# Performance work log

Hardware: AMD Instinct MI355X
Metric: run time of the kernel (lower is better)

Reference implementation:

```python
import jax, jax.numpy as jnp
import numpy as np

SIZE = 1024
CODE_DIM = 256
B, H, W = 32, 32, 32


def setup_inputs() -> dict:
    key = jax.random.key(0)
    k1, k2 = jax.random.split(key)
    z = jax.random.normal(k1, (B, CODE_DIM, H, W), dtype=jnp.float32)
    embeddings = jax.random.normal(k2, (SIZE, CODE_DIM), dtype=jnp.float32)
    return {"z": z, "embeddings": embeddings}


def reference(z, embeddings):
    b, c, h, w = z.shape  # c == code_dim
    # (b, h, w, c) -> (N, c)
    flat = jnp.transpose(z, (0, 2, 3, 1)).reshape(-1, c)
    d = (
        jnp.sum(flat * flat, axis=-1, keepdims=True)
        - 2.0 * (flat @ embeddings.T)
        + jnp.sum(embeddings * embeddings, axis=-1)
    )
    idx = jnp.argmin(d, axis=-1)  # (N,)
    quantized = embeddings[idx].reshape(b, h, w, c)
    quantized = jnp.transpose(quantized, (0, 3, 1, 2))  # (b, c, h, w)
    straight_through = jax.lax.stop_gradient(quantized - z) + z
    return quantized, straight_through, idx.reshape(b, h, w)
```

## Files before the change

### kernel.cpp

```cpp
#include <hip/hip_runtime.h>

#define NPTS   32768
#define NCODES 1024
#define DIM    256
#define HWSZ   1024
#define CHW    (DIM*HWSZ)
#define QSZ    8388608

typedef __attribute__((ext_vector_type(8))) short short8;
typedef __attribute__((ext_vector_type(4))) float f32x4;

__device__ __forceinline__ void gload16(const void* g, void* l) {
    __builtin_amdgcn_global_load_lds((const __attribute__((address_space(1))) void*)g,
                                     (__attribute__((address_space(3))) void*)l,
                                     16, 0, 0);
}

__device__ __forceinline__ unsigned bf16_rne(float f) {
    unsigned u = __float_as_uint(f);
    return (u + 0x7fffu + ((u >> 16) & 1u)) >> 16;
}

__device__ __forceinline__ unsigned long long pack_di(float d, int code) {
    unsigned u = __float_as_uint(d);
    unsigned key = u ^ ((unsigned)((int)u >> 31) | 0x80000000u);
    return ((unsigned long long)key << 32) | (unsigned)code;
}

__device__ __forceinline__ int fmoff(int n, int c) {
    return ((((((n >> 7) * 2 + ((n >> 6) & 1)) * 8 + (c >> 5)) * 4 + ((n >> 4) & 3)) * 4
             + ((c >> 3) & 3)) * 16 + (n & 15)) * 8 + (c & 7);
}

__global__ void k_prep(const float* __restrict__ z, const float* __restrict__ emb,
                       short* __restrict__ Xh, short* __restrict__ Xl,
                       short* __restrict__ Eh, short* __restrict__ El,
                       float* __restrict__ e2, unsigned long long* __restrict__ win) {
    int tid = threadIdx.x;
    if (blockIdx.x >= 2048) {
        int eb = blockIdx.x - 2048;
        int widx = eb * 256 + tid;
        if (widx < NPTS) win[widx] = ~0ull;
        int lane = tid & 63, w = tid >> 6;
        int k = eb * 4 + w;
        const float4 v = *reinterpret_cast<const float4*>(emb + k * DIM + lane * 4);
        float f[4] = {v.x, v.y, v.z, v.w};
        short h[4], l[4];
        double s = 0.0;
        #pragma unroll
        for (int i = 0; i < 4; ++i) {
            unsigned hb = bf16_rne(f[i]);
            float hf = __uint_as_float(hb << 16);
            h[i] = (short)hb;
            l[i] = (short)bf16_rne(f[i] - hf);
            s += (double)f[i] * f[i];
        }
        int eoff = fmoff(k, lane * 4);
        *reinterpret_cast<short4*>(Eh + eoff) = make_short4(h[0], h[1], h[2], h[3]);
        *reinterpret_cast<short4*>(El + eoff) = make_short4(l[0], l[1], l[2], l[3]);
        #pragma unroll
        for (int m = 32; m >= 1; m >>= 1) s += __shfl_xor(s, m);
        if (lane == 0) e2[k] = (float)s;
        return;
    }
    __shared__ float T[64][33];
    int blk = blockIdx.x;
    int b   = blk >> 6;
    int rem = blk & 63;
    int ht  = rem >> 1;
    int ch  = rem & 1;
    int hw0 = ht * 32;
    int n0  = b * HWSZ + hw0;
    int hq = tid & 7, cr = tid >> 3;
    int wp = tid >> 3, wc = tid & 7;
    const float* zp = z + b * CHW;
    #pragma unroll
    for (int cc2 = 0; cc2 < 2; ++cc2) {
        int c0 = (ch * 2 + cc2) * 64;
        if (cc2) __syncthreads();
        #pragma unroll
        for (int p = 0; p < 2; ++p) {
            int c = p * 32 + cr;
            float4 v = *reinterpret_cast<const float4*>(zp + (c0 + c) * HWSZ + hw0 + hq * 4);
            T[c][hq * 4 + 0] = v.x; T[c][hq * 4 + 1] = v.y;
            T[c][hq * 4 + 2] = v.z; T[c][hq * 4 + 3] = v.w;
        }
        __syncthreads();
        short8 hv, lv;
        #pragma unroll
        for (int k = 0; k < 8; ++k) {
            float f = T[wc * 8 + k][wp];
            unsigned hb = bf16_rne(f);
            float hf = __uint_as_float(hb << 16);
            hv[k] = (short)hb;
            lv[k] = (short)bf16_rne(f - hf);
        }
        int off = fmoff(n0 + wp, c0 + wc * 8);
        *reinterpret_cast<short8*>(Xh + off) = hv;
        *reinterpret_cast<short8*>(Xl + off) = lv;
    }
}

__launch_bounds__(256, 3)
__global__ void k_dist(const short* __restrict__ Xh, const short* __restrict__ Xl,
                       const short* __restrict__ Eh, const short* __restrict__ El,
                       const float* __restrict__ e2, unsigned long long* __restrict__ win) {
    __shared__ __align__(16) short Bs[2][8192];
    __shared__ float sv[2][128];
    __shared__ int   si[2][128];

    const int tid = threadIdx.x;
    const int pt = blockIdx.x & 255;
    const int ct = blockIdx.x >> 8;
    const int n0 = pt * 128;
    const int c0 = ct * 128;

    const int w = tid >> 6, lane = tid & 63;
    const int wr = w >> 1, wc = w & 1;
    const int m16 = lane & 15, quad = lane >> 4;

    f32x4 acc[4][4];
    #pragma unroll
    for (int i = 0; i < 4; ++i)
        #pragma unroll
        for (int j = 0; j < 4; ++j) acc[i][j] = (f32x4){0.f, 0.f, 0.f, 0.f};

    const short* Ahb = Xh + (pt * 2 + wr) * 16384 + lane * 8;
    const short* Alb = Xl + (pt * 2 + wr) * 16384 + lane * 8;
    const short* Ebase = (w < 2 ? Eh : El) + (ct * 2 + wc) * 16384 + lane * 8;
    char* BsW0 = (char*)&Bs[0][0] + w * 4096;
    char* BsW1 = (char*)&Bs[1][0] + w * 4096;

    #define STAGE_B(buf, tt) do {                                       \
        char* d_ = (buf) ? BsW1 : BsW0;                                 \
        const short* s_ = Ebase + (tt) * 2048;                          \
        gload16(s_,        d_);                                         \
        gload16(s_ + 512,  d_ + 1024);                                  \
        gload16(s_ + 1024, d_ + 2048);                                  \
        gload16(s_ + 1536, d_ + 3072);                                  \
    } while (0)

    short8 ah[2][4], al[4];
    STAGE_B(0, 0);
    #pragma unroll
    for (int i = 0; i < 4; ++i)
        ah[0][i] = *reinterpret_cast<const short8*>(Ahb + i * 512);

    #pragma unroll
    for (int t = 0; t < 8; ++t) {
        const int cur = t & 1;
        __builtin_amdgcn_s_barrier();
        #pragma unroll
        for (int i = 0; i < 4; ++i)
            al[i] = *reinterpret_cast<const short8*>(Alb + t * 2048 + i * 512);
        if (t < 7) STAGE_B(cur ^ 1, t + 1);
        if (t < 7) asm volatile("s_waitcnt vmcnt(8)" ::: "memory");
        else       asm volatile("s_waitcnt vmcnt(4)" ::: "memory");
        __builtin_amdgcn_sched_barrier(0);

        short8 bh[4];
        #pragma unroll
        for (int j = 0; j < 4; ++j)
            bh[j] = *(const short8*)&Bs[cur][(wc * 4 + j) * 512 + lane * 8];
        #pragma unroll
        for (int i = 0; i < 4; ++i)
            #pragma unroll
            for (int j = 0; j < 4; ++j)
                acc[i][j] = __builtin_amdgcn_mfma_f32_16x16x32_bf16(ah[cur][i], bh[j], acc[i][j], 0, 0, 0);
        #pragma unroll
        for (int i = 0; i < 4; ++i)
            #pragma unroll
            for (int j = 0; j < 4; ++j)
                acc[i][j] = __builtin_amdgcn_mfma_f32_16x16x32_bf16(al[i], bh[j], acc[i][j], 0, 0, 0);
        if (t < 7) {
            #pragma unroll
            for (int i = 0; i < 4; ++i)
                ah[cur ^ 1][i] = *reinterpret_cast<const short8*>(Ahb + (t + 1) * 2048 + i * 512);
        }
        short8 bl[4];
        #pragma unroll
        for (int j = 0; j < 4; ++j)
            bl[j] = *(const short8*)&Bs[cur][(8 + wc * 4 + j) * 512 + lane * 8];
        #pragma unroll
        for (int i = 0; i < 4; ++i)
            #pragma unroll
            for (int j = 0; j < 4; ++j)
                acc[i][j] = __builtin_amdgcn_mfma_f32_16x16x32_bf16(ah[cur][i], bl[j], acc[i][j], 0, 0, 0);
    }
    #undef STAGE_B

    float ecol[4];
    #pragma unroll
    for (int j = 0; j < 4; ++j) ecol[j] = e2[c0 + wc * 64 + j * 16 + m16];

    #pragma unroll
    for (int i = 0; i < 4; ++i) {
        #pragma unroll
        for (int rr = 0; rr < 4; ++rr) {
            float best = 3.4e38f; int bi = 0;
            #pragma unroll
            for (int j = 0; j < 4; ++j) {
                float d = fmaf(-2.f, acc[i][j][rr], ecol[j]);
                int code = c0 + wc * 64 + j * 16 + m16;
                if (d < best) { best = d; bi = code; }
            }
            #pragma unroll
            for (int m = 1; m < 16; m <<= 1) {
                float ov = __shfl_xor(best, m);
                int   oi = __shfl_xor(bi, m);
                if (ov < best || (ov == best && oi < bi)) { best = ov; bi = oi; }
            }
            if (m16 == 0) {
                int p = wr * 64 + i * 16 + quad * 4 + rr;
                sv[wc][p] = best; si[wc][p] = bi;
            }
        }
    }
    __syncthreads();
    if (tid < 128) {
        float v0 = sv[0][tid]; int i0 = si[0][tid];
        float v1 = sv[1][tid]; int i1 = si[1][tid];
        if (v1 < v0) { v0 = v1; i0 = i1; }
        atomicMin(win + n0 + tid, pack_di(v0, i0));
    }
}

__global__ void k_out(const float* __restrict__ z, const float* __restrict__ emb,
                      const unsigned long long* __restrict__ win,
                      float* __restrict__ out) {
    __shared__ float Q[32][129];
    __shared__ int sbi[32];
    int blk = blockIdx.x;
    int n0 = (blk >> 1) * 32;
    int ch = blk & 1;
    int tid = threadIdx.x;
    if (tid < 32) {
        int n = n0 + tid;
        int bi = (int)(unsigned)(win[n] & 0xFFFFFFFFull);
        sbi[tid] = bi;
        if (ch == 0) out[2 * QSZ + n] = (float)bi;
    }
    __syncthreads();
    {
        int pt = tid >> 3, co = tid & 7;
        const float* ep = emb + sbi[pt] * DIM + ch * 128;
        #pragma unroll
        for (int j = 0; j < 4; ++j) {
            int c = j * 32 + co * 4;
            float4 v = *reinterpret_cast<const float4*>(ep + c);
            Q[pt][c] = v.x; Q[pt][c + 1] = v.y; Q[pt][c + 2] = v.z; Q[pt][c + 3] = v.w;
        }
    }
    __syncthreads();
    int hq = tid & 7, cr = tid >> 3;
    int b = n0 >> 10, hw0 = (n0 & 1023) + hq * 4;
    #pragma unroll
    for (int it = 0; it < 4; ++it) {
        int cl = it * 32 + cr;
        int c  = ch * 128 + cl;
        int off = b * CHW + c * HWSZ + hw0;
        float4 zv = *reinterpret_cast<const float4*>(z + off);
        float4 q = make_float4(Q[hq * 4 + 0][cl], Q[hq * 4 + 1][cl],
                               Q[hq * 4 + 2][cl], Q[hq * 4 + 3][cl]);
        *reinterpret_cast<float4*>(out + off) = q;
        float4 st = make_float4((q.x - zv.x) + zv.x, (q.y - zv.y) + zv.y,
                                (q.z - zv.z) + zv.z, (q.w - zv.w) + zv.w);
        *reinterpret_cast<float4*>(out + QSZ + off) = st;
    }
}

extern "C" void kernel_launch(void* const* d_in, const int* in_sizes, int n_in,
                              void* d_out, int out_size, void* d_ws, size_t ws_size,
                              hipStream_t stream) {
    const float* z   = (const float*)d_in[0];
    const float* emb = (const float*)d_in[1];
    float* out = (float*)d_out;
    float* ws  = (float*)d_ws;

    short* Eh   = (short*)ws;
    short* El   = (short*)(ws + 131072);
    float* e2   = ws + 262144;
    unsigned long long* win = (unsigned long long*)(ws + 263168);

    short* Xh = (short*)out;
    short* Xl = (short*)(out + 4194304);

    hipLaunchKernelGGL(k_prep, dim3(2304), dim3(256), 0, stream, z, emb, Xh, Xl, Eh, El, e2, win);
    hipLaunchKernelGGL(k_dist, dim3(2048), dim3(256), 0, stream, Xh, Xl, Eh, El, e2, win);
    hipLaunchKernelGGL(k_out,  dim3(2048), dim3(256), 0, stream, z, emb, win, out);
}
```

Baseline: 165.8 us.

## Switch distance GEMM to 32x32x16 MFMA with matching fragment layout

Measured after the change: 194.7 us. +17.4%, slower.

```diff
diff --git a/kernel.cpp b/kernel.cpp
--- a/kernel.cpp
+++ b/kernel.cpp
@@ -8,7 +8,7 @@
 #define QSZ    8388608
 
 typedef __attribute__((ext_vector_type(8))) short short8;
-typedef __attribute__((ext_vector_type(4))) float f32x4;
+typedef __attribute__((ext_vector_type(16))) float f32x16;
 
 __device__ __forceinline__ void gload16(const void* g, void* l) {
     __builtin_amdgcn_global_load_lds((const __attribute__((address_space(1))) void*)g,
@@ -27,9 +27,8 @@
     return ((unsigned long long)key << 32) | (unsigned)code;
 }
 
-__device__ __forceinline__ int fmoff(int n, int c) {
-    return ((((((n >> 7) * 2 + ((n >> 6) & 1)) * 8 + (c >> 5)) * 4 + ((n >> 4) & 3)) * 4
-             + ((c >> 3) & 3)) * 16 + (n & 15)) * 8 + (c & 7);
+__device__ __forceinline__ int fmoff32(int n, int c) {
+    return ((n >> 5) * 16 + (c >> 4)) * 512 + (((c >> 3) & 1) * 32 + (n & 31)) * 8 + (c & 7);
 }
 
 __global__ void k_prep(const float* __restrict__ z, const float* __restrict__ emb,
@@ -55,7 +54,7 @@
             l[i] = (short)bf16_rne(f[i] - hf);
             s += (double)f[i] * f[i];
         }
-        int eoff = fmoff(k, lane * 4);
+        int eoff = fmoff32(k, lane * 4);
         *reinterpret_cast<short4*>(Eh + eoff) = make_short4(h[0], h[1], h[2], h[3]);
         *reinterpret_cast<short4*>(El + eoff) = make_short4(l[0], l[1], l[2], l[3]);
         #pragma unroll
@@ -95,7 +94,7 @@
             hv[k] = (short)hb;
             lv[k] = (short)bf16_rne(f - hf);
         }
-        int off = fmoff(n0 + wp, c0 + wc * 8);
+        int off = fmoff32(n0 + wp, c0 + wc * 8);
         *reinterpret_cast<short8*>(Xh + off) = hv;
         *reinterpret_cast<short8*>(Xl + off) = lv;
     }
@@ -117,101 +116,121 @@
 
     const int w = tid >> 6, lane = tid & 63;
     const int wr = w >> 1, wc = w & 1;
-    const int m16 = lane & 15, quad = lane >> 4;
-
-    f32x4 acc[4][4];
-    #pragma unroll
-    for (int i = 0; i < 4; ++i)
-        #pragma unroll
-        for (int j = 0; j < 4; ++j) acc[i][j] = (f32x4){0.f, 0.f, 0.f, 0.f};
-
-    const short* Ahb = Xh + (pt * 2 + wr) * 16384 + lane * 8;
-    const short* Alb = Xl + (pt * 2 + wr) * 16384 + lane * 8;
-    const short* Ebase = (w < 2 ? Eh : El) + (ct * 2 + wc) * 16384 + lane * 8;
-    char* BsW0 = (char*)&Bs[0][0] + w * 4096;
-    char* BsW1 = (char*)&Bs[1][0] + w * 4096;
-
-    #define STAGE_B(buf, tt) do {                                       \
-        char* d_ = (buf) ? BsW1 : BsW0;                                 \
-        const short* s_ = Ebase + (tt) * 2048;                          \
-        gload16(s_,        d_);                                         \
-        gload16(s_ + 512,  d_ + 1024);                                  \
-        gload16(s_ + 1024, d_ + 2048);                                  \
-        gload16(s_ + 1536, d_ + 3072);                                  \
+    const int l31 = lane & 31, lh = lane >> 5;
+
+    f32x16 acc[2][2];
+    #pragma unroll
+    for (int i = 0; i < 2; ++i)
+        #pragma unroll
+        for (int j = 0; j < 2; ++j)
+            #pragma unroll
+            for (int e = 0; e < 16; ++e) acc[i][j][e] = 0.f;
+
+    const short* Ahb = Xh + (pt * 4 + wr * 2) * 8192 + lane * 8;
+    const short* Alb = Xl + (pt * 4 + wr * 2) * 8192 + lane * 8;
+    const short* Ebase = (w < 2 ? Eh : El) + (ct * 4 + (w & 1) * 2) * 8192 + lane * 8;
+    char* Bd0 = (char*)&Bs[0][0] + ((w >> 1) * 8 + (w & 1) * 4) * 1024;
+    char* Bd1 = (char*)&Bs[1][0] + ((w >> 1) * 8 + (w & 1) * 4) * 1024;
+
+    #define STAGE_B(buf, tt) do {                                     \
+        char* d_ = (buf) ? Bd1 : Bd0;                                 \
+        const short* s_ = Ebase + (tt) * 1024;                        \
+        gload16(s_,              d_);                                 \
+        gload16(s_ + 512,        d_ + 1024);                          \
+        gload16(s_ + 8192,       d_ + 2048);                          \
+        gload16(s_ + 8192 + 512, d_ + 3072);                          \
     } while (0)
 
     short8 ah[2][4], al[4];
     STAGE_B(0, 0);
-    #pragma unroll
-    for (int i = 0; i < 4; ++i)
-        ah[0][i] = *reinterpret_cast<const short8*>(Ahb + i * 512);
+    __builtin_amdgcn_sched_barrier(0);
+    #pragma unroll
+    for (int f = 0; f < 4; ++f)
+        ah[0][f] = *reinterpret_cast<const short8*>(Ahb + (f >> 1) * 8192 + (f & 1) * 512);
+    asm volatile("s_waitcnt vmcnt(4)" ::: "memory");
+    __builtin_amdgcn_s_barrier();
+    __builtin_amdgcn_sched_barrier(0);
 
     #pragma unroll
     for (int t = 0; t < 8; ++t) {
         const int cur = t & 1;
-        __builtin_amdgcn_s_barrier();
-        #pragma unroll
-        for (int i = 0; i < 4; ++i)
-            al[i] = *reinterpret_cast<const short8*>(Alb + t * 2048 + i * 512);
+        short8 bh[4];
+        #pragma unroll
+        for (int f = 0; f < 4; ++f)
+            bh[f] = *(const short8*)&Bs[cur][(wc * 4 + f) * 512 + lane * 8];
+        #pragma unroll
+        for (int f = 0; f < 4; ++f)
+            al[f] = *reinterpret_cast<const short8*>(Alb + (f >> 1) * 8192 + (t * 2 + (f & 1)) * 512);
         if (t < 7) STAGE_B(cur ^ 1, t + 1);
-        if (t < 7) asm volatile("s_waitcnt vmcnt(8)" ::: "memory");
-        else       asm volatile("s_waitcnt vmcnt(4)" ::: "memory");
-        __builtin_amdgcn_sched_barrier(0);
-
-        short8 bh[4];
-        #pragma unroll
-        for (int j = 0; j < 4; ++j)
-            bh[j] = *(const short8*)&Bs[cur][(wc * 4 + j) * 512 + lane * 8];
-        #pragma unroll
-        for (int i = 0; i < 4; ++i)
-            #pragma unroll
-            for (int j = 0; j < 4; ++j)
-                acc[i][j] = __builtin_amdgcn_mfma_f32_16x16x32_bf16(ah[cur][i], bh[j], acc[i][j], 0, 0, 0);
-        #pragma unroll
-        for (int i = 0; i < 4; ++i)
-            #pragma unroll
-            for (int j = 0; j < 4; ++j)
-                acc[i][j] = __builtin_amdgcn_mfma_f32_16x16x32_bf16(al[i], bh[j], acc[i][j], 0, 0, 0);
+
+        __builtin_amdgcn_s_setprio(1);
+        #pragma unroll
+        for (int i2 = 0; i2 < 2; ++i2)
+            #pragma unroll
+            for (int j2 = 0; j2 < 2; ++j2)
+                #pragma unroll
+                for (int kf = 0; kf < 2; ++kf)
+                    acc[i2][j2] = __builtin_amdgcn_mfma_f32_32x32x16_bf16(
+                        ah[cur][i2 * 2 + kf], bh[j2 * 2 + kf], acc[i2][j2], 0, 0, 0);
+        #pragma unroll
+        for (int i2 = 0; i2 < 2; ++i2)
+            #pragma unroll
+            for (int j2 = 0; j2 < 2; ++j2)
+                #pragma unroll
+                for (int kf = 0; kf < 2; ++kf)
+                    acc[i2][j2] = __builtin_amdgcn_mfma_f32_32x32x16_bf16(
+                        al[i2 * 2 + kf], bh[j2 * 2 + kf], acc[i2][j2], 0, 0, 0);
+        __builtin_amdgcn_s_setprio(0);
         if (t < 7) {
-            #pragma unroll
-            for (int i = 0; i < 4; ++i)
-                ah[cur ^ 1][i] = *reinterpret_cast<const short8*>(Ahb + (t + 1) * 2048 + i * 512);
+            __builtin_amdgcn_sched_barrier(0);
+            #pragma unroll
+            for (int f = 0; f < 4; ++f)
+                ah[cur ^ 1][f] = *reinterpret_cast<const short8*>(
+                    Ahb + (f >> 1) * 8192 + ((t + 1) * 2 + (f & 1)) * 512);
         }
         short8 bl[4];
         #pragma unroll
-        for (int j = 0; j < 4; ++j)
-            bl[j] = *(const short8*)&Bs[cur][(8 + wc * 4 + j) * 512 + lane * 8];
-        #pragma unroll
-        for (int i = 0; i < 4; ++i)
-            #pragma unroll
-            for (int j = 0; j < 4; ++j)
-                acc[i][j] = __builtin_amdgcn_mfma_f32_16x16x32_bf16(ah[cur][i], bl[j], acc[i][j], 0, 0, 0);
+        for (int f = 0; f < 4; ++f)
+            bl[f] = *(const short8*)&Bs[cur][(8 + wc * 4 + f) * 512 + lane * 8];
+        __builtin_amdgcn_s_setprio(1);
+        #pragma unroll
+        for (int i2 = 0; i2 < 2; ++i2)
+            #pragma unroll
+            for (int j2 = 0; j2 < 2; ++j2)
+                #pragma unroll
+                for (int kf = 0; kf < 2; ++kf)
+                    acc[i2][j2] = __builtin_amdgcn_mfma_f32_32x32x16_bf16(
+                        ah[cur][i2 * 2 + kf], bl[j2 * 2 + kf], acc[i2][j2], 0, 0, 0);
+        __builtin_amdgcn_s_setprio(0);
+        if (t < 7) {
+            asm volatile("s_waitcnt vmcnt(4)" ::: "memory");
+            __builtin_amdgcn_s_barrier();
+            __builtin_amdgcn_sched_barrier(0);
+        }
     }
     #undef STAGE_B
 
-    float ecol[4];
-    #pragma unroll
-    for (int j = 0; j < 4; ++j) ecol[j] = e2[c0 + wc * 64 + j * 16 + m16];
-
-    #pragma unroll
-    for (int i = 0; i < 4; ++i) {
-        #pragma unroll
-        for (int rr = 0; rr < 4; ++rr) {
-            float best = 3.4e38f; int bi = 0;
-            #pragma unroll
-            for (int j = 0; j < 4; ++j) {
-                float d = fmaf(-2.f, acc[i][j][rr], ecol[j]);
-                int code = c0 + wc * 64 + j * 16 + m16;
-                if (d < best) { best = d; bi = code; }
-            }
-            #pragma unroll
-            for (int m = 1; m < 16; m <<= 1) {
+    float ecol[2];
+    ecol[0] = e2[c0 + wc * 64 + l31];
+    ecol[1] = e2[c0 + wc * 64 + 32 + l31];
+    const int codeb = c0 + wc * 64 + l31;
+
+    #pragma unroll
+    for (int i2 = 0; i2 < 2; ++i2) {
+        #pragma unroll
+        for (int r = 0; r < 16; ++r) {
+            float d0 = fmaf(-2.f, acc[i2][0][r], ecol[0]);
+            float d1 = fmaf(-2.f, acc[i2][1][r], ecol[1]);
+            float best = d0; int bi = codeb;
+            if (d1 < best) { best = d1; bi = codeb + 32; }
+            #pragma unroll
+            for (int m = 1; m < 32; m <<= 1) {
                 float ov = __shfl_xor(best, m);
                 int   oi = __shfl_xor(bi, m);
                 if (ov < best || (ov == best && oi < bi)) { best = ov; bi = oi; }
             }
-            if (m16 == 0) {
-                int p = wr * 64 + i * 16 + quad * 4 + rr;
+            if (l31 == 0) {
+                int p = wr * 64 + i2 * 32 + (r & 3) + 8 * (r >> 2) + 4 * lh;
                 sv[wc][p] = best; si[wc][p] = bi;
             }
         }
```
